# Optimization experiments

Measured on AMD Instinct MI355X. Metric: run time of the kernel, lower is better.

Reference implementation:

```python
import jax, jax.numpy as jnp
import numpy as np

N_NODES = 50000
N_EDGES = 800000
IN_CH = 256
HID = 256
OUT_CH = 128


def setup_inputs() -> dict:
    key = jax.random.key(0)
    ks = jax.random.split(key, 12)
    x = jax.random.normal(ks[0], (N_NODES, IN_CH), dtype=jnp.float32)
    adj_rows = jnp.sort(jax.random.randint(ks[1], (N_EDGES,), 0, N_NODES, dtype=jnp.int32))
    adj_cols = jax.random.randint(ks[2], (N_EDGES,), 0, N_NODES, dtype=jnp.int32)
    # normalized adjacency weights (~1/degree scale)
    adj_vals = jax.random.uniform(ks[3], (N_EDGES,), dtype=jnp.float32) / 16.0
    def xavier(k, fan_in, fan_out):
        lim = float(np.sqrt(6.0 / (fan_in + fan_out)))
        return jax.random.uniform(k, (fan_in, fan_out), dtype=jnp.float32, minval=-lim, maxval=lim)
    Wa0 = xavier(ks[4], IN_CH, HID)
    Wa1 = xavier(ks[5], HID, HID)
    Wl0 = xavier(ks[6], IN_CH + HID, HID)
    Wl1 = xavier(ks[7], 2 * HID, OUT_CH)
    return {
        'x': x, 'adj_rows': adj_rows, 'adj_cols': adj_cols, 'adj_vals': adj_vals,
        'Wa0': Wa0, 'ba0': jnp.zeros((HID,), jnp.float32),
        'Wa1': Wa1, 'ba1': jnp.zeros((HID,), jnp.float32),
        'Wl0': Wl0, 'bl0': jnp.zeros((HID,), jnp.float32),
        'Wl1': Wl1, 'bl1': jnp.zeros((OUT_CH,), jnp.float32),
    }


def reference(x, adj_rows, adj_cols, adj_vals, Wa0, ba0, Wa1, ba1, Wl0, bl0, Wl1, bl1):
    n = x.shape[0]

    def spmm(h):
        # sparse adj @ h : gather neighbor rows, scale by edge weight, segment-sum into dst
        return jax.ops.segment_sum(adj_vals[:, None] * h[adj_cols], adj_rows, num_segments=n)

    # layer 0
    agg = jax.nn.relu(spmm(x) @ Wa0 + ba0)
    h = jax.nn.relu(jnp.concatenate((x, agg), axis=1) @ Wl0 + bl0)
    # layer 1 (last: no activation after linear)
    agg = jax.nn.relu(spmm(h) @ Wa1 + ba1)
    h = jnp.concatenate((h, agg), axis=1) @ Wl1 + bl1
    # F.normalize: row-wise L2 with eps=1e-12
    norm = jnp.maximum(jnp.linalg.norm(h, axis=1, keepdims=True), 1e-12)
    return h / norm
```

## Files before the change

kernel.cpp:

```cpp
#include <hip/hip_runtime.h>

typedef unsigned short u16;
typedef __attribute__((ext_vector_type(8))) __bf16 bf16x8;
typedef __attribute__((ext_vector_type(4))) float f32x4;
typedef __attribute__((ext_vector_type(8))) u16 u16x8;
typedef __attribute__((ext_vector_type(4))) u16 u16x4;

__device__ __forceinline__ float bf2f(u16 u) {
  return __builtin_bit_cast(float, ((unsigned)u) << 16);
}
__device__ __forceinline__ u16 f2bf(float f) {
  unsigned x = __builtin_bit_cast(unsigned, f);
  x += 0x7fffu + ((x >> 16) & 1u);
  return (u16)(x >> 16);
}
__device__ __forceinline__ f32x4 cvt4(u16x4 v) {
  return (f32x4){bf2f(v.x), bf2f(v.y), bf2f(v.z), bf2f(v.w)};
}
__device__ __forceinline__ void gload_lds16(const void* g, void* l) {
  __builtin_amdgcn_global_load_lds(
      (const __attribute__((address_space(1))) void*)g,
      (__attribute__((address_space(3))) void*)l, 16, 0, 0);
}

__global__ void prepw4_kernel(const float* __restrict__ W0, u16* __restrict__ T0,
                              const float* __restrict__ W1, u16* __restrict__ T1,
                              const float* __restrict__ W2, u16* __restrict__ T2,
                              const float* __restrict__ W3, u16* __restrict__ T3) {
  int i = blockIdx.x * 256 + threadIdx.x;
  const float* W; u16* T; int K, N;
  if (i < 65536)        { W = W0; T = T0; K = 256; N = 256; }
  else if (i < 131072)  { W = W1; T = T1; K = 256; N = 256; i -= 65536; }
  else if (i < 262144)  { W = W2; T = T2; K = 512; N = 256; i -= 131072; }
  else if (i < 327680)  { W = W3; T = T3; K = 512; N = 128; i -= 262144; }
  else return;
  int k = i / N, n = i - k * N;
  T[(size_t)n * K + k] = f2bf(W[i]);
}

__global__ void cvtx_kernel(const float* __restrict__ in, u16* __restrict__ out,
                            int total4) {
  int i = blockIdx.x * 256 + threadIdx.x;
  if (i >= total4) return;
  const float4 v = ((const float4*)in)[i];
  u16x4 o = { f2bf(v.x), f2bf(v.y), f2bf(v.z), f2bf(v.w) };
  ((u16x4*)out)[i] = o;
}

__global__ void rowptr_kernel(const int* __restrict__ rows, int nE,
                              int* __restrict__ rp, int nN) {
  int i = blockIdx.x * 256 + threadIdx.x;
  if (i > nN) return;
  int lo = 0, hi = nE;
  while (lo < hi) { int mid = (lo + hi) >> 1; if (rows[mid] < i) lo = mid + 1; else hi = mid; }
  rp[i] = lo;
}

__global__ __launch_bounds__(128) void spmm_kernel(
    const u16* __restrict__ X, const int* __restrict__ rp,
    const int* __restrict__ cols, const float* __restrict__ vals,
    u16* __restrict__ out, int nN) {
  int lane = threadIdx.x & 63;
  int node = blockIdx.x * 2 + (threadIdx.x >> 6);
  if (node >= nN) return;
  int e0 = rp[node], e1 = rp[node + 1];
  f32x4 s0 = {0.f, 0.f, 0.f, 0.f}, s1 = s0, s2 = s0, s3 = s0;
  const u16* xp = X + (size_t)lane * 4;
  int e = e0;
  for (; e + 8 <= e1; e += 8) {
    int c[8]; float v[8]; u16x4 xv[8];
    #pragma unroll
    for (int i = 0; i < 8; ++i) { c[i] = cols[e + i]; v[i] = vals[e + i]; }
    #pragma unroll
    for (int i = 0; i < 8; ++i) xv[i] = *(const u16x4*)(xp + (size_t)c[i] * 256);
    s0 += v[0] * cvt4(xv[0]); s1 += v[1] * cvt4(xv[1]);
    s2 += v[2] * cvt4(xv[2]); s3 += v[3] * cvt4(xv[3]);
    s0 += v[4] * cvt4(xv[4]); s1 += v[5] * cvt4(xv[5]);
    s2 += v[6] * cvt4(xv[6]); s3 += v[7] * cvt4(xv[7]);
  }
  if (e + 4 <= e1) {
    int c0 = cols[e], c1 = cols[e + 1], c2 = cols[e + 2], c3 = cols[e + 3];
    float v0 = vals[e], v1 = vals[e + 1], v2 = vals[e + 2], v3 = vals[e + 3];
    u16x4 x0 = *(const u16x4*)(xp + (size_t)c0 * 256);
    u16x4 x1 = *(const u16x4*)(xp + (size_t)c1 * 256);
    u16x4 x2 = *(const u16x4*)(xp + (size_t)c2 * 256);
    u16x4 x3 = *(const u16x4*)(xp + (size_t)c3 * 256);
    s0 += v0 * cvt4(x0); s1 += v1 * cvt4(x1);
    s2 += v2 * cvt4(x2); s3 += v3 * cvt4(x3);
    e += 4;
  }
  for (; e < e1; ++e) {
    int c = cols[e];
    float v = vals[e];
    s0 += v * cvt4(*(const u16x4*)(xp + (size_t)c * 256));
  }
  f32x4 s = (s0 + s1) + (s2 + s3);
  u16x4 o = { f2bf(s.x), f2bf(s.y), f2bf(s.z), f2bf(s.w) };
  *(u16x4*)(out + (size_t)node * 256 + lane * 4) = o;
}

template<int KTOT, bool SPLIT, bool RELU, bool OUTF32, bool NORM, int NB>
__global__ __launch_bounds__(256) void gemm_kernel(
    const u16* __restrict__ A0, const u16* __restrict__ A1,
    const u16* __restrict__ Wt, const float* __restrict__ bias,
    void* __restrict__ outp, int M, int N) {
  __shared__ u16 As[2][128 * 64];
  __shared__ u16 Bs[2][128 * 64];
  __shared__ float red[128][2];

  const int lane = threadIdx.x & 63;
  const int wid = threadIdx.x >> 6;
  const int wr = wid >> 1, wc = wid & 1;

  int row0b, col0b;
  if (NB == 2) {
    const int b = blockIdx.x;
    const int g = b >> 4, w = b & 15;
    const int nfull = gridDim.x >> 4;
    int pair, col;
    if (g < nfull) { pair = g * 8 + (w & 7); col = w >> 3; }
    else { int rem = b - (nfull << 4); pair = nfull * 8 + (rem >> 1); col = rem & 1; }
    row0b = pair * 128; col0b = col * 128;
  } else {
    row0b = blockIdx.x * 128; col0b = 0;
  }

  const int lr = lane & 15;
  const int kg = lane >> 4;

  const int u = (wid * 4) * 64 + lane;

  auto stage = [&](int buf, int kt) {
    const u16* Asrc = (!SPLIT || kt < 4) ? A0 : A1;
    const int kkl = (!SPLIT || kt < 4) ? kt * 64 : (kt - 4) * 64;
    #pragma unroll
    for (int i = 0; i < 4; ++i) {
      const int c = wid * 4 + i;
      const int uu = u + i * 64;
      const int row = uu >> 3;
      const int ksd = uu & 7;
      const int kss = ksd ^ (row & 7);
      int grow = row0b + row;
      if (grow >= M) grow = M - 1;
      gload_lds16(Asrc + (size_t)grow * 256 + kkl + kss * 8, &As[buf][c * 512]);
      gload_lds16(Wt + (size_t)(col0b + row) * KTOT + kt * 64 + kss * 8, &Bs[buf][c * 512]);
    }
  };

  f32x4 acc[4][4];
  #pragma unroll
  for (int ni = 0; ni < 4; ++ni) {
    float bv = bias[col0b + wc * 64 + ni * 16 + lr];
    #pragma unroll
    for (int mi = 0; mi < 4; ++mi) acc[mi][ni] = (f32x4){bv, bv, bv, bv};
  }

  constexpr int KSTEPS = KTOT / 64;
  stage(0, 0);
  __syncthreads();

  for (int kt = 0; kt < KSTEPS; ++kt) {
    const int cur = kt & 1;
    if (kt + 1 < KSTEPS) stage(cur ^ 1, kt + 1);

    #pragma unroll
    for (int ks = 0; ks < 2; ++ks) {
      const int q = ks * 4 + kg;
      bf16x8 a[4], b[4];
      #pragma unroll
      for (int mi = 0; mi < 4; ++mi) {
        const int r = wr * 64 + mi * 16 + lr;
        a[mi] = __builtin_bit_cast(bf16x8,
            *(const u16x8*)&As[cur][r * 64 + (q ^ (r & 7)) * 8]);
      }
      #pragma unroll
      for (int ni = 0; ni < 4; ++ni) {
        const int cb = wc * 64 + ni * 16 + lr;
        b[ni] = __builtin_bit_cast(bf16x8,
            *(const u16x8*)&Bs[cur][cb * 64 + (q ^ (cb & 7)) * 8]);
      }
      #pragma unroll
      for (int mi = 0; mi < 4; ++mi)
        #pragma unroll
        for (int ni = 0; ni < 4; ++ni)
          acc[mi][ni] = __builtin_amdgcn_mfma_f32_16x16x32_bf16(a[mi], b[ni], acc[mi][ni], 0, 0, 0);
    }
    __syncthreads();
  }

  float invn[4][4];
  if (NORM) {
    #pragma unroll
    for (int mi = 0; mi < 4; ++mi) {
      #pragma unroll
      for (int j = 0; j < 4; ++j) {
        float p = 0.f;
        #pragma unroll
        for (int ni = 0; ni < 4; ++ni) { float v = acc[mi][ni][j]; p += v * v; }
        #pragma unroll
        for (int m = 1; m < 16; m <<= 1) p += __shfl_xor(p, m, 64);
        int rl = wr * 64 + mi * 16 + kg * 4 + j;
        if (lr == 0) red[rl][wc] = p;
        invn[mi][j] = 0.f;
      }
    }
    __syncthreads();
    #pragma unroll
    for (int mi = 0; mi < 4; ++mi) {
      #pragma unroll
      for (int j = 0; j < 4; ++j) {
        int rl = wr * 64 + mi * 16 + kg * 4 + j;
        float ss = red[rl][0] + red[rl][1];
        float nrm = sqrtf(ss);
        nrm = nrm > 1e-12f ? nrm : 1e-12f;
        invn[mi][j] = 1.f / nrm;
      }
    }
  }

  #pragma unroll
  for (int mi = 0; mi < 4; ++mi) {
    #pragma unroll
    for (int j = 0; j < 4; ++j) {
      int r = row0b + wr * 64 + mi * 16 + kg * 4 + j;
      if (r >= M) continue;
      #pragma unroll
      for (int ni = 0; ni < 4; ++ni) {
        float v = acc[mi][ni][j];
        if (RELU) v = v > 0.f ? v : 0.f;
        if (NORM) v *= invn[mi][j];
        int c = col0b + wc * 64 + ni * 16 + lr;
        if (OUTF32) ((float*)outp)[(size_t)r * N + c] = v;
        else        ((u16*)outp)[(size_t)r * N + c] = f2bf(v);
      }
    }
  }
}

extern "C" void kernel_launch(void* const* d_in, const int* in_sizes, int n_in,
                              void* d_out, int out_size, void* d_ws, size_t ws_size,
                              hipStream_t stream) {
  const float* x        = (const float*)d_in[0];
  const int*   adj_rows = (const int*)d_in[1];
  const int*   adj_cols = (const int*)d_in[2];
  const float* adj_vals = (const float*)d_in[3];
  const float* Wa0 = (const float*)d_in[4];
  const float* ba0 = (const float*)d_in[5];
  const float* Wa1 = (const float*)d_in[6];
  const float* ba1 = (const float*)d_in[7];
  const float* Wl0 = (const float*)d_in[8];
  const float* bl0 = (const float*)d_in[9];
  const float* Wl1 = (const float*)d_in[10];
  const float* bl1 = (const float*)d_in[11];

  const int nN = in_sizes[0] / 256;
  const int nE = in_sizes[1];

  char* ws = (char*)d_ws;
  size_t off = 0;
  auto alloc = [&](size_t bytes) -> void* {
    void* p = ws + off;
    off += (bytes + 255) & ~(size_t)255;
    return p;
  };
  u16* x_bf  = (u16*)alloc((size_t)nN * 256 * 2);
  u16* aggA  = (u16*)alloc((size_t)nN * 256 * 2);
  u16* aggB  = (u16*)alloc((size_t)nN * 256 * 2);
  u16* h_bf  = (u16*)alloc((size_t)nN * 256 * 2);
  int* rp    = (int*)alloc((size_t)(nN + 1) * 4);
  u16* wt_a0 = (u16*)alloc(256 * 256 * 2);
  u16* wt_a1 = (u16*)alloc(256 * 256 * 2);
  u16* wt_l0 = (u16*)alloc(512 * 256 * 2);
  u16* wt_l1 = (u16*)alloc(512 * 128 * 2);
  if (off > ws_size) return;

  dim3 blk(256);
  prepw4_kernel<<<dim3(1280), blk, 0, stream>>>(Wa0, wt_a0, Wa1, wt_a1, Wl0, wt_l0, Wl1, wt_l1);
  cvtx_kernel<<<dim3((nN * 64 + 255) / 256), blk, 0, stream>>>(x, x_bf, nN * 64);
  rowptr_kernel<<<dim3((nN + 1 + 255) / 256), blk, 0, stream>>>(adj_rows, nE, rp, nN);

  const int MB = (nN + 127) / 128;
  dim3 gN256(2 * MB);
  dim3 gN128(MB);
  dim3 gNode((nN + 1) / 2);
  dim3 sblk(128);

  spmm_kernel<<<gNode, sblk, 0, stream>>>(x_bf, rp, adj_cols, adj_vals, aggA, nN);
  gemm_kernel<256, false, true, false, false, 2><<<gN256, blk, 0, stream>>>(aggA, nullptr, wt_a0, ba0, aggB, nN, 256);
  gemm_kernel<512, true, true, false, false, 2><<<gN256, blk, 0, stream>>>(x_bf, aggB, wt_l0, bl0, h_bf, nN, 256);
  spmm_kernel<<<gNode, sblk, 0, stream>>>(h_bf, rp, adj_cols, adj_vals, aggA, nN);
  gemm_kernel<256, false, true, false, false, 2><<<gN256, blk, 0, stream>>>(aggA, nullptr, wt_a1, ba1, aggB, nN, 256);
  gemm_kernel<512, true, false, true, true, 1><<<gN128, blk, 0, stream>>>(h_bf, aggB, wt_l1, bl1, (float*)d_out, nN, 128);
}
```

Before: 217.2 us.

## Halve GEMM row tile to 64 and merge prep kernels into one launch

The GEMM kernel now uses 64-row output tiles instead of 128, with each wave computing 32x64. This doubles the block count for better occupancy and CU balance on the ~50k-row problem. The cost is reloading B tiles more often, so weight reuse per block drops. The weight transpose, x conversion and row-pointer kernels are also merged into one launch to cut launch overhead.

```diff
diff --git a/kernel.cpp b/kernel.cpp
--- a/kernel.cpp
+++ b/kernel.cpp
@@ -23,33 +23,36 @@
       (__attribute__((address_space(3))) void*)l, 16, 0, 0);
 }
 
-__global__ void prepw4_kernel(const float* __restrict__ W0, u16* __restrict__ T0,
-                              const float* __restrict__ W1, u16* __restrict__ T1,
-                              const float* __restrict__ W2, u16* __restrict__ T2,
-                              const float* __restrict__ W3, u16* __restrict__ T3) {
-  int i = blockIdx.x * 256 + threadIdx.x;
-  const float* W; u16* T; int K, N;
-  if (i < 65536)        { W = W0; T = T0; K = 256; N = 256; }
-  else if (i < 131072)  { W = W1; T = T1; K = 256; N = 256; i -= 65536; }
-  else if (i < 262144)  { W = W2; T = T2; K = 512; N = 256; i -= 131072; }
-  else if (i < 327680)  { W = W3; T = T3; K = 512; N = 128; i -= 262144; }
-  else return;
-  int k = i / N, n = i - k * N;
-  T[(size_t)n * K + k] = f2bf(W[i]);
-}
-
-__global__ void cvtx_kernel(const float* __restrict__ in, u16* __restrict__ out,
-                            int total4) {
-  int i = blockIdx.x * 256 + threadIdx.x;
-  if (i >= total4) return;
-  const float4 v = ((const float4*)in)[i];
-  u16x4 o = { f2bf(v.x), f2bf(v.y), f2bf(v.z), f2bf(v.w) };
-  ((u16x4*)out)[i] = o;
-}
-
-__global__ void rowptr_kernel(const int* __restrict__ rows, int nE,
-                              int* __restrict__ rp, int nN) {
-  int i = blockIdx.x * 256 + threadIdx.x;
+__global__ void prep_kernel(const float* __restrict__ x, u16* __restrict__ x_bf, int cvtxBlocks,
+                            const float* __restrict__ W0, u16* __restrict__ T0,
+                            const float* __restrict__ W1, u16* __restrict__ T1,
+                            const float* __restrict__ W2, u16* __restrict__ T2,
+                            const float* __restrict__ W3, u16* __restrict__ T3,
+                            const int* __restrict__ rows, int nE, int* __restrict__ rp, int nN) {
+  int b = blockIdx.x;
+  if (b < cvtxBlocks) {
+    int i = b * 256 + threadIdx.x;
+    if (i >= nN * 64) return;
+    const float4 v = ((const float4*)x)[i];
+    u16x4 o = { f2bf(v.x), f2bf(v.y), f2bf(v.z), f2bf(v.w) };
+    ((u16x4*)x_bf)[i] = o;
+    return;
+  }
+  b -= cvtxBlocks;
+  if (b < 1280) {
+    int i = b * 256 + threadIdx.x;
+    const float* W; u16* T; int K, N;
+    if (i < 65536)        { W = W0; T = T0; K = 256; N = 256; }
+    else if (i < 131072)  { W = W1; T = T1; K = 256; N = 256; i -= 65536; }
+    else if (i < 262144)  { W = W2; T = T2; K = 512; N = 256; i -= 131072; }
+    else if (i < 327680)  { W = W3; T = T3; K = 512; N = 128; i -= 262144; }
+    else return;
+    int k = i / N, n = i - k * N;
+    T[(size_t)n * K + k] = f2bf(W[i]);
+    return;
+  }
+  b -= 1280;
+  int i = b * 256 + threadIdx.x;
   if (i > nN) return;
   int lo = 0, hi = nE;
   while (lo < hi) { int mid = (lo + hi) >> 1; if (rows[mid] < i) lo = mid + 1; else hi = mid; }
@@ -104,9 +107,9 @@
     const u16* __restrict__ A0, const u16* __restrict__ A1,
     const u16* __restrict__ Wt, const float* __restrict__ bias,
     void* __restrict__ outp, int M, int N) {
-  __shared__ u16 As[2][128 * 64];
+  __shared__ u16 As[2][64 * 64];
   __shared__ u16 Bs[2][128 * 64];
-  __shared__ float red[128][2];
+  __shared__ float red[64][2];
 
   const int lane = threadIdx.x & 63;
   const int wid = threadIdx.x >> 6;
@@ -120,39 +123,43 @@
     int pair, col;
     if (g < nfull) { pair = g * 8 + (w & 7); col = w >> 3; }
     else { int rem = b - (nfull << 4); pair = nfull * 8 + (rem >> 1); col = rem & 1; }
-    row0b = pair * 128; col0b = col * 128;
+    row0b = pair * 64; col0b = col * 128;
   } else {
-    row0b = blockIdx.x * 128; col0b = 0;
+    row0b = blockIdx.x * 64; col0b = 0;
   }
 
   const int lr = lane & 15;
   const int kg = lane >> 4;
-
-  const int u = (wid * 4) * 64 + lane;
 
   auto stage = [&](int buf, int kt) {
     const u16* Asrc = (!SPLIT || kt < 4) ? A0 : A1;
     const int kkl = (!SPLIT || kt < 4) ? kt * 64 : (kt - 4) * 64;
     #pragma unroll
-    for (int i = 0; i < 4; ++i) {
-      const int c = wid * 4 + i;
-      const int uu = u + i * 64;
+    for (int i = 0; i < 2; ++i) {
+      const int ca = wid * 2 + i;
+      const int uu = ca * 64 + lane;
       const int row = uu >> 3;
-      const int ksd = uu & 7;
-      const int kss = ksd ^ (row & 7);
+      const int kss = (uu & 7) ^ (row & 7);
       int grow = row0b + row;
       if (grow >= M) grow = M - 1;
-      gload_lds16(Asrc + (size_t)grow * 256 + kkl + kss * 8, &As[buf][c * 512]);
-      gload_lds16(Wt + (size_t)(col0b + row) * KTOT + kt * 64 + kss * 8, &Bs[buf][c * 512]);
+      gload_lds16(Asrc + (size_t)grow * 256 + kkl + kss * 8, &As[buf][ca * 512]);
+    }
+    #pragma unroll
+    for (int i = 0; i < 4; ++i) {
+      const int cb = wid * 4 + i;
+      const int uu = cb * 64 + lane;
+      const int row = uu >> 3;
+      const int kss = (uu & 7) ^ (row & 7);
+      gload_lds16(Wt + (size_t)(col0b + row) * KTOT + kt * 64 + kss * 8, &Bs[buf][cb * 512]);
     }
   };
 
-  f32x4 acc[4][4];
+  f32x4 acc[2][4];
   #pragma unroll
   for (int ni = 0; ni < 4; ++ni) {
     float bv = bias[col0b + wc * 64 + ni * 16 + lr];
     #pragma unroll
-    for (int mi = 0; mi < 4; ++mi) acc[mi][ni] = (f32x4){bv, bv, bv, bv};
+    for (int mi = 0; mi < 2; ++mi) acc[mi][ni] = (f32x4){bv, bv, bv, bv};
   }
 
   constexpr int KSTEPS = KTOT / 64;
@@ -166,10 +173,10 @@
     #pragma unroll
     for (int ks = 0; ks < 2; ++ks) {
       const int q = ks * 4 + kg;
-      bf16x8 a[4], b[4];
-      #pragma unroll
-      for (int mi = 0; mi < 4; ++mi) {
-        const int r = wr * 64 + mi * 16 + lr;
+      bf16x8 a[2], b[4];
+      #pragma unroll
+      for (int mi = 0; mi < 2; ++mi) {
+        const int r = wr * 32 + mi * 16 + lr;
         a[mi] = __builtin_bit_cast(bf16x8,
             *(const u16x8*)&As[cur][r * 64 + (q ^ (r & 7)) * 8]);
       }
@@ -180,7 +187,7 @@
             *(const u16x8*)&Bs[cur][cb * 64 + (q ^ (cb & 7)) * 8]);
       }
       #pragma unroll
-      for (int mi = 0; mi < 4; ++mi)
+      for (int mi = 0; mi < 2; ++mi)
         #pragma unroll
         for (int ni = 0; ni < 4; ++ni)
           acc[mi][ni] = __builtin_amdgcn_mfma_f32_16x16x32_bf16(a[mi], b[ni], acc[mi][ni], 0, 0, 0);
@@ -188,10 +195,10 @@
     __syncthreads();
   }
 
-  float invn[4][4];
+  float invn[2][4];
   if (NORM) {
     #pragma unroll
-    for (int mi = 0; mi < 4; ++mi) {
+    for (int mi = 0; mi < 2; ++mi) {
       #pragma unroll
       for (int j = 0; j < 4; ++j) {
         float p = 0.f;
@@ -199,17 +206,17 @@
         for (int ni = 0; ni < 4; ++ni) { float v = acc[mi][ni][j]; p += v * v; }
         #pragma unroll
         for (int m = 1; m < 16; m <<= 1) p += __shfl_xor(p, m, 64);
-        int rl = wr * 64 + mi * 16 + kg * 4 + j;
+        int rl = wr * 32 + mi * 16 + kg * 4 + j;
         if (lr == 0) red[rl][wc] = p;
         invn[mi][j] = 0.f;
       }
     }
     __syncthreads();
     #pragma unroll
-    for (int mi = 0; mi < 4; ++mi) {
+    for (int mi = 0; mi < 2; ++mi) {
       #pragma unroll
       for (int j = 0; j < 4; ++j) {
-        int rl = wr * 64 + mi * 16 + kg * 4 + j;
+        int rl = wr * 32 + mi * 16 + kg * 4 + j;
         float ss = red[rl][0] + red[rl][1];
         float nrm = sqrtf(ss);
         nrm = nrm > 1e-12f ? nrm : 1e-12f;
@@ -219,10 +226,10 @@
   }
 
   #pragma unroll
-  for (int mi = 0; mi < 4; ++mi) {
+  for (int mi = 0; mi < 2; ++mi) {
     #pragma unroll
     for (int j = 0; j < 4; ++j) {
-      int r = row0b + wr * 64 + mi * 16 + kg * 4 + j;
+      int r = row0b + wr * 32 + mi * 16 + kg * 4 + j;
       if (r >= M) continue;
       #pragma unroll
       for (int ni = 0; ni < 4; ++ni) {
@@ -275,11 +282,13 @@
   if (off > ws_size) return;
 
   dim3 blk(256);
-  prepw4_kernel<<<dim3(1280), blk, 0, stream>>>(Wa0, wt_a0, Wa1, wt_a1, Wl0, wt_l0, Wl1, wt_l1);
-  cvtx_kernel<<<dim3((nN * 64 + 255) / 256), blk, 0, stream>>>(x, x_bf, nN * 64);
-  rowptr_kernel<<<dim3((nN + 1 + 255) / 256), blk, 0, stream>>>(adj_rows, nE, rp, nN);
-
-  const int MB = (nN + 127) / 128;
+  const int cvtxBlocks = (nN * 64 + 255) / 256;
+  const int rpBlocks = (nN + 1 + 255) / 256;
+  prep_kernel<<<dim3(cvtxBlocks + 1280 + rpBlocks), blk, 0, stream>>>(
+      x, x_bf, cvtxBlocks, Wa0, wt_a0, Wa1, wt_a1, Wl0, wt_l0, Wl1, wt_l1,
+      adj_rows, nE, rp, nN);
+
+  const int MB = (nN + 63) / 64;
   dim3 gN256(2 * MB);
   dim3 gN128(MB);
   dim3 gNode((nN + 1) / 2);
```

New measurement: 221.7 us. 1.02x slower.
